# Performance work log

Hardware: AMD Instinct MI355X
Metric: run time of the kernel (lower is better)

The kernel has to match this reference:

```python
import jax, jax.numpy as jnp
import numpy as np

# ---- constants (match init_kwargs / input_specs) ----
B, NPG, EPG = 512, 50, 60          # graphs, nodes/graph, edges/graph
D, V = 128, 100000                 # embedding_dim, num_items
SPLITS, SCALE = 4, 12.0            # euler steps, logit scale
N, E = B * NPG, B * EPG
STDV = 1.0 / np.sqrt(D)


def _seg_sum(vals, idx, n):
    return jax.ops.segment_sum(vals, idx, num_segments=n)


def _l2norm(x, eps=1e-12):
    return x / jnp.maximum(jnp.linalg.norm(x, axis=-1, keepdims=True), eps)


def setup_inputs() -> dict:
    key = jax.random.key(0)
    ks = jax.random.split(key, 40)
    u = lambda i, shape: jax.random.uniform(ks[i], shape, minval=-STDV, maxval=STDV, dtype=jnp.float32)
    offs = jnp.repeat(jnp.arange(B, dtype=jnp.int32) * NPG, EPG)
    inp = dict(
        iid=jax.random.randint(ks[0], (N,), 0, V),
        src=jax.random.randint(ks[1], (E,), 0, NPG).astype(jnp.int32) + offs,
        dst=jax.random.randint(ks[2], (E,), 0, NPG).astype(jnp.int32) + offs,
        edge_w=jax.random.uniform(ks[3], (E,), minval=0.1, maxval=1.0, dtype=jnp.float32),
        edge_t=jax.random.uniform(ks[4], (E,), dtype=jnp.float32),
        node_t=jax.random.uniform(ks[5], (N,), dtype=jnp.float32),
        emb=u(6, (V, D)),
        # GGNN layer (num_layers=1): W1, W2 and torch-layout GRUCell(2D -> D)
        W1=u(7, (D, D)), W2=u(8, (D, D)),
        gw_ih=u(9, (3 * D, 2 * D)), gw_hh=u(10, (3 * D, D)),
        gb_ih=u(11, (3 * D,)), gb_hh=u(12, (3 * D,)),
        # GraphGRUODE GCNConv weights (x@W + b), norm='both'
        Wxr=u(13, (D, D)), bxr=u(14, (D,)), Wxz=u(15, (D, D)), bxz=u(16, (D,)),
        Wxh=u(17, (D, D)), bxh=u(18, (D,)), Whr=u(19, (D, D)), bhr=u(20, (D,)),
        Whz=u(21, (D, D)), bhz=u(22, (D,)), Whh=u(23, (D, D)), bhh=u(24, (D,)),
        # AttnReadout
        Wu=u(25, (D, D)), Wv=u(26, (D, D)), bv=u(27, (D,)), We=u(28, (D, 1)),
        # fc_sr: [2D -> D], no bias
        W_sr=u(29, (2 * D, D)),
    )
    return inp


def reference(iid, src, dst, edge_w, edge_t, node_t, emb,
              W1, W2, gw_ih, gw_hh, gb_ih, gb_hh,
              Wxr, bxr, Wxz, bxz, Wxh, bxh, Whr, bhr, Whz, bhz, Whh, bhh,
              Wu, Wv, bv, We, W_sr):
    # ---- embedding + normalize ----
    feat = _l2norm(emb[iid])                                   # [N, D]

    # ---- GGNNLayer: weighted mean over in-edges, both directions, GRU cell ----
    wcol = edge_w[:, None]
    num1 = _seg_sum(feat[src] * wcol, dst, N)
    den1 = _seg_sum(edge_w, dst, N)
    neigh1 = num1 / jnp.where(den1 == 0, 1.0, den1)[:, None]    # zero for isolated nodes
    num2 = _seg_sum(feat[dst] * wcol, src, N)
    den2 = _seg_sum(edge_w, src, N)
    neigh2 = num2 / jnp.where(den2 == 0, 1.0, den2)[:, None]
    hn = jnp.concatenate([neigh1 @ W1, neigh2 @ W2], axis=1)    # [N, 2D]
    gi = hn @ gw_ih.T + gb_ih
    gh = feat @ gw_hh.T + gb_hh
    ir, iz, ig = jnp.split(gi, 3, axis=1)
    hr, hz, hg = jnp.split(gh, 3, axis=1)
    r = jax.nn.sigmoid(ir + hr)
    z = jax.nn.sigmoid(iz + hz)
    g = jnp.tanh(ig + r * hg)
    feat = (1.0 - z) * g + z * feat
    feat = _l2norm(feat)

    # ---- GraphGRUODE: euler integration over dynamic masked subgraphs ----
    x = feat
    t_end = edge_t.max()
    dt = t_end / SPLITS
    nodiag = src != dst

    def ode_f(t, h):
        nm = node_t >= t                                        # node subgraph mask
        em = (edge_t <= t) & nm[src] & nm[dst] & nodiag          # edge mask (no self-loops)
        emf = em.astype(h.dtype)
        deg = _seg_sum(emf, src, N) + _seg_sum(emf, dst, N)      # undirected degree (reverse edges added)
        dis = jnp.clip(deg, 1.0, None) ** -0.5

        def conv(inp, W, b):                                     # GCNConv, norm='both'
            s = inp * dis[:, None]
            agg = (_seg_sum(s[src] * emf[:, None], dst, N)
                   + _seg_sum(s[dst] * emf[:, None], src, N))
            return (agg * dis[:, None]) @ W + b

        rr = jax.nn.sigmoid(conv(x, Wxr, bxr) + conv(h, Whr, bhr))
        zz = jax.nn.sigmoid(conv(x, Wxz, bxz) + conv(h, Whz, bhz))
        uu = jnp.tanh(conv(x, Wxh, bxh) + conv(rr * h, Whh, bhh))
        dh = (1.0 - zz) * (uu - h)
        return jnp.where(nm[:, None], dh, 0.0)

    h = x
    for k in range(SPLITS):
        h = h + dt * ode_f(k * dt, h)
    feat = _l2norm(h)

    # ---- AttnReadout (fixed NPG nodes/graph -> reshape as segment ops) ----
    fb = feat.reshape(B, NPG, D)
    last = fb[:, -1, :]                                          # last node of each session
    e = jax.nn.sigmoid(fb @ Wu + (last @ Wv + bv)[:, None, :]) @ We   # [B, NPG, 1]
    alpha = jax.nn.softmax(e, axis=1)
    sr_g = jnp.sum(fb * alpha, axis=1)                           # [B, D]

    sr = _l2norm(jnp.concatenate([last, sr_g], axis=1) @ W_sr)   # [B, D]
    target = _l2norm(emb)                                        # [V, D]
    logits = sr @ target.T                                       # [B, V]
    return jax.nn.log_softmax(SCALE * logits, axis=-1)
```

## Files before the change

kernel.cpp:

```cpp
#include <hip/hip_runtime.h>

#define BB 512
#define NPG 50
#define EPG 60
#define DD 128
#define VV 100000
#define VPAD 100032
#define NSPLITS 4
#define FSCALE 12.0f
#define NN (BB*NPG)
#define EE (BB*EPG)
#define NCB (VPAD/64)
#define HSTR 132
#define RSTR 136
#define TSTR 72
#define MSTR 72

typedef __attribute__((ext_vector_type(8))) short bfx8;
typedef __attribute__((ext_vector_type(4))) float f32x4;

__device__ __forceinline__ float sigmoidf_(float x){ return 1.f/(1.f+expf(-x)); }
__device__ __forceinline__ short f2bf(float f){
  union { float f; unsigned u; } v; v.f = f;
  unsigned r = v.u + 0x7FFF + ((v.u >> 16) & 1);
  return (short)(r >> 16);
}
__device__ __forceinline__ float bf2f(short s){
  union { unsigned u; float f; } v; v.u = ((unsigned)(unsigned short)s) << 16;
  return v.f;
}
__device__ __forceinline__ unsigned cvtpk_(float lo, float hi){
  unsigned r; asm("v_cvt_pk_bf16_f32 %0, %1, %2" : "=v"(r) : "v"(lo), "v"(hi)); return r;
}
__device__ __forceinline__ bfx8 pack8(float4 a, float4 b){
  union { bfx8 v; unsigned u[4]; } w;
  w.u[0] = cvtpk_(a.x, a.y); w.u[1] = cvtpk_(a.z, a.w);
  w.u[2] = cvtpk_(b.x, b.y); w.u[3] = cvtpk_(b.z, b.w);
  return w.v;
}

__global__ __launch_bounds__(256) void k_embn(const float* __restrict__ emb, short* __restrict__ embn) {
  int row = blockIdx.x*4 + (threadIdx.x >> 6);
  int lane = threadIdx.x & 63;
  if (row >= VPAD) return;
  if (row >= VV) { embn[(size_t)row*DD+lane]=0; embn[(size_t)row*DD+64+lane]=0; return; }
  const float* r = emb + (size_t)row*DD;
  float a = r[lane], b = r[lane+64];
  float s = a*a + b*b;
  for (int off=32; off; off>>=1) s += __shfl_down(s, off);
  s = __shfl(s, 0);
  float inv = 1.0f/fmaxf(sqrtf(s), 1e-12f);
  embn[(size_t)row*DD+lane]    = f2bf(a*inv);
  embn[(size_t)row*DD+64+lane] = f2bf(b*inv);
}

__global__ __launch_bounds__(128) void k_gather(const int* __restrict__ iid, const float* __restrict__ emb,
                                                float* __restrict__ x, short* __restrict__ xb) {
  int n = blockIdx.x, d = threadIdx.x;
  int v = iid[n];
  float e = emb[(size_t)v*DD + d];
  __shared__ float red2[2];
  float ss = e*e;
  for (int off=32; off; off>>=1) ss += __shfl_down(ss, off);
  if ((d & 63)==0) red2[d>>6] = ss;
  __syncthreads();
  float inv = 1.f/fmaxf(sqrtf(red2[0]+red2[1]), 1e-12f);
  float f = e*inv;
  x[(size_t)n*DD + d] = f;
  xb[(size_t)n*DD + d] = f2bf(f);
}

__global__ __launch_bounds__(256) void k_dt(const float* __restrict__ edge_t, float* __restrict__ dtp) {
  __shared__ float red[256];
  float m = -1e30f;
  for (int e = threadIdx.x; e < EE; e += 256) m = fmaxf(m, edge_t[e]);
  red[threadIdx.x] = m; __syncthreads();
  for (int s=128; s; s>>=1){ if ((int)threadIdx.x < s) red[threadIdx.x] = fmaxf(red[threadIdx.x], red[threadIdx.x+s]); __syncthreads(); }
  if (threadIdx.x==0) dtp[0] = red[0] / (float)NSPLITS;
}

__global__ void k_m12t(const float* __restrict__ W1, const float* __restrict__ W2,
                       const float* __restrict__ gw_ih, short* __restrict__ M12t) {
  int c = blockIdx.x, k = threadIdx.x;
  const float* Wrow = (k < 128) ? (W1 + (size_t)k*128) : (W2 + (size_t)(k-128)*128);
  const float* grow = gw_ih + (size_t)c*256 + ((k < 128) ? 0 : 128);
  float s = 0.f;
  for (int j = 0; j < 128; ++j) s += Wrow[j]*grow[j];
  M12t[(size_t)c*256 + k] = f2bf(s);
}
__global__ void k_bfcopy(const float* __restrict__ src, short* __restrict__ dst) {
  size_t i = (size_t)blockIdx.x*blockDim.x + threadIdx.x;
  dst[i] = f2bf(src[i]);
}
__global__ void k_whrzt(const float* __restrict__ Whr, const float* __restrict__ Whz,
                        short* __restrict__ Whrzt) {
  int c = blockIdx.x, k = threadIdx.x;
  float v = (c < 128) ? Whr[(size_t)k*128 + c] : Whz[(size_t)k*128 + (c-128)];
  Whrzt[(size_t)c*128 + k] = f2bf(v);
}
__global__ void k_w3t(const float* __restrict__ Wxr, const float* __restrict__ Wxz,
                      const float* __restrict__ Wxh, short* __restrict__ W3t) {
  int c = blockIdx.x, k = threadIdx.x;
  float v = (c < 128) ? Wxr[(size_t)k*128 + c]
          : (c < 256) ? Wxz[(size_t)k*128 + (c-128)]
                      : Wxh[(size_t)k*128 + (c-256)];
  W3t[(size_t)c*128 + k] = f2bf(v);
}
__global__ void k_wt128(const float* __restrict__ W, short* __restrict__ Wt) {
  int c = blockIdx.x, k = threadIdx.x;
  Wt[(size_t)c*128 + k] = f2bf(W[(size_t)k*128 + c]);
}
__global__ void k_build_bias(const float* __restrict__ bxr, const float* __restrict__ bhr,
                             const float* __restrict__ bxz, const float* __restrict__ bhz,
                             const float* __restrict__ bxh, const float* __restrict__ bhh,
                             float* __restrict__ brz, float* __restrict__ bu) {
  int t = threadIdx.x;
  if (t < 128) brz[t] = bxr[t] + bhr[t];
  else if (t < 256) brz[t] = bxz[t-128] + bhz[t-128];
  else bu[t-256] = bxh[t-256] + bhh[t-256];
}

__global__ __launch_bounds__(256) void k_grp_mean(const int* __restrict__ src, const int* __restrict__ dst,
                                                  const float* __restrict__ ew, const float* __restrict__ feat,
                                                  short* __restrict__ ABb) {
  __shared__ float fl[NPG*128];
  __shared__ float n1[NPG*128];
  __shared__ float n2[NPG*128];
  __shared__ int sl[EPG], tl[EPG];
  __shared__ float wl[EPG];
  __shared__ float d1[NPG], d2[NPG];
  int b = blockIdx.x, tid = threadIdx.x;
  int nb = b*NPG, eb = b*EPG;
  for (int i = tid; i < NPG*32; i += 256) {
    ((float4*)fl)[i] = ((const float4*)(feat + (size_t)nb*128))[i];
    ((float4*)n1)[i] = make_float4(0.f,0.f,0.f,0.f);
    ((float4*)n2)[i] = make_float4(0.f,0.f,0.f,0.f);
  }
  if (tid < EPG) { sl[tid] = src[eb+tid]-nb; tl[tid] = dst[eb+tid]-nb; wl[tid] = ew[eb+tid]; }
  __syncthreads();
  const int dgrp = tid >> 7, d = tid & 127;
  if (dgrp == 0) {
    for (int e = 0; e < EPG; ++e) n1[tl[e]*128+d] += fl[sl[e]*128+d]*wl[e];
  } else {
    for (int e = 0; e < EPG; ++e) n2[sl[e]*128+d] += fl[tl[e]*128+d]*wl[e];
  }
  if (tid < NPG) {
    float den = 0.f;
    for (int e = 0; e < EPG; ++e) den += (tl[e]==tid) ? wl[e] : 0.f;
    d1[tid] = (den == 0.f) ? 1.f : den;
  } else if (tid >= 128 && tid < 128+NPG) {
    int dd = tid - 128;
    float den = 0.f;
    for (int e = 0; e < EPG; ++e) den += (sl[e]==dd) ? wl[e] : 0.f;
    d2[dd] = (den == 0.f) ? 1.f : den;
  }
  __syncthreads();
  for (int n = 0; n < NPG; ++n) {
    float v = dgrp ? (n2[n*128+d]/d2[n]) : (n1[n*128+d]/d1[n]);
    ABb[(size_t)(nb+n)*256 + dgrp*128 + d] = f2bf(v);
  }
}

__global__ __launch_bounds__(128) void k_gru(const float* __restrict__ gi, const float* __restrict__ gh,
                                             float* __restrict__ x, short* __restrict__ xb2) {
  int n = blockIdx.x, d = threadIdx.x;
  const float* gin = gi + (size_t)n*384;
  const float* ghn = gh + (size_t)n*384;
  float ir = gin[d], iz = gin[128+d], ig = gin[256+d];
  float hr = ghn[d], hz = ghn[128+d], hg = ghn[256+d];
  float f0 = x[(size_t)n*DD + d];
  float r = sigmoidf_(ir + hr);
  float z = sigmoidf_(iz + hz);
  float g = tanhf(ig + r*hg);
  float f = (1.f - z)*g + z*f0;
  __shared__ float red2[2];
  float ss = f*f;
  for (int off=32; off; off>>=1) ss += __shfl_down(ss, off);
  if ((d & 63)==0) red2[d>>6] = ss;
  __syncthreads();
  float inv = 1.f/fmaxf(sqrtf(red2[0]+red2[1]), 1e-12f);
  float out = f*inv;
  x[(size_t)n*DD + d] = out;
  xb2[(size_t)n*DD + d] = f2bf(out);
}

__global__ __launch_bounds__(512, 4) void k_ode_fused(
    const int* __restrict__ src, const int* __restrict__ dst,
    const float* __restrict__ edge_t, const float* __restrict__ node_t,
    const float* __restrict__ dtp,
    float* __restrict__ x, short* __restrict__ fbb,
    const short* __restrict__ XA,
    const short* __restrict__ Whrzt, const short* __restrict__ Whht,
    const float* __restrict__ brz, const float* __restrict__ bu)
{
  __shared__ __align__(16) float hl[NPG*HSTR];
  __shared__ __align__(16) short rhb[NPG*RSTR];
  __shared__ __align__(16) short T1t[128*TSTR];
  __shared__ __align__(16) short Mp[64*MSTR];
  __shared__ int   rp[NPG+1];
  __shared__ short ci[2*EPG];
  __shared__ int   cnt[NPG];
  __shared__ int   stl[EPG];
  __shared__ float etl[EPG];
  __shared__ float ntl[NPG];
  __shared__ float disl[NPG];
  __shared__ unsigned long long actm_s;
  __shared__ float red8[8];

  const int b = blockIdx.x, tid = threadIdx.x;
  const int nb = b*NPG, eb = b*EPG;
  const int wave = tid>>6, lane = tid&63, quad = lane>>4, l16 = lane&15;
  const float dtv = dtp[0];

  for (int i = tid; i < NPG*32; i += 512) {
    int n = i >> 5, dq = i & 31;
    ((float4*)(hl + n*HSTR))[dq] = ((const float4*)(x + (size_t)(nb+n)*128))[dq];
  }
  if (tid < EPG) { stl[tid] = (src[eb+tid]-nb) | ((dst[eb+tid]-nb)<<16); etl[tid] = edge_t[eb+tid]; }
  if (tid >= 64 && tid < 64+NPG) ntl[tid-64] = node_t[nb+tid-64];
  __syncthreads();

  if (tid < NPG) {
    int c = 0;
    for (int e = 0; e < EPG; ++e) { int st=stl[e]; int s=st&0xffff, t=st>>16; c += (s==tid)+(t==tid); }
    cnt[tid] = c;
  }
  __syncthreads();
  if (tid == 0) { int a = 0; for (int n = 0; n < NPG; ++n) { rp[n] = a; a += cnt[n]; } rp[NPG] = a; }
  __syncthreads();
  if (tid < NPG) {
    int w = rp[tid];
    for (int e = 0; e < EPG; ++e) {
      int st = stl[e]; int s = st & 0xffff, t = st >> 16;
      if (t == tid) ci[w++] = (short)(s | (e<<8));
      if (s == tid) ci[w++] = (short)(t | (e<<8));
    }
  }
  __syncthreads();

  float zreg[4][4];

#define HW_PHASE(WT, XAOFS, USERH)                                                   \
  {                                                                                  \
    f32x4 acc[4] = {{0.f,0.f,0.f,0.f},{0.f,0.f,0.f,0.f},{0.f,0.f,0.f,0.f},{0.f,0.f,0.f,0.f}}; \
    const int coln = wave*16 + l16;                                                  \
    _Pragma("unroll")                                                                \
    for (int k0 = 0; k0 < 128; k0 += 32) {                                           \
      bfx8 af[4];                                                                    \
      _Pragma("unroll")                                                              \
      for (int m = 0; m < 4; ++m) {                                                  \
        int arow = m*16 + l16; if (arow > NPG-1) arow = NPG-1;                       \
        if (USERH) {                                                                 \
          af[m] = *(const bfx8*)&rhb[arow*RSTR + k0 + quad*8];                       \
        } else {                                                                     \
          const float* hp = &hl[arow*HSTR + k0 + quad*8];                            \
          float4 f0 = *(const float4*)hp;                                            \
          float4 f1 = *(const float4*)(hp+4);                                        \
          af[m] = pack8(f0, f1);                                                     \
        }                                                                            \
      }                                                                              \
      bfx8 bfr = *(const bfx8*)&(WT)[(size_t)coln*128 + k0 + quad*8];                \
      _Pragma("unroll")                                                              \
      for (int m = 0; m < 4; ++m)                                                    \
        acc[m] = __builtin_amdgcn_mfma_f32_16x16x32_bf16(af[m], bfr, acc[m], 0, 0, 0); \
    }                                                                                \
    _Pragma("unroll")                                                                \
    for (int m = 0; m < 4; ++m)                                                      \
      _Pragma("unroll")                                                              \
      for (int r = 0; r < 4; ++r) {                                                  \
        int row = m*16 + quad*4 + r;                                                 \
        int crow = (row > NPG-1) ? (NPG-1) : row;                                    \
        float v = acc[m][r] + bf2f(XA[(size_t)(nb+crow)*384 + (XAOFS) + coln]);      \
        T1t[coln*TSTR + row] = f2bf(v);                                              \
      }                                                                              \
  }

#define AGG_PHASE(WHICH)                                                             \
  {                                                                                  \
    f32x4 acc[4] = {{0.f,0.f,0.f,0.f},{0.f,0.f,0.f,0.f},{0.f,0.f,0.f,0.f},{0.f,0.f,0.f,0.f}}; \
    const int cold = wave*16 + l16;                                                  \
    _Pragma("unroll")                                                                \
    for (int k0 = 0; k0 < 64; k0 += 32) {                                            \
      bfx8 af[4];                                                                    \
      _Pragma("unroll")                                                              \
      for (int m = 0; m < 4; ++m) af[m] = *(const bfx8*)&Mp[(m*16+l16)*MSTR + k0 + quad*8]; \
      bfx8 bfr = *(const bfx8*)&T1t[cold*TSTR + k0 + quad*8];                        \
      _Pragma("unroll")                                                              \
      for (int m = 0; m < 4; ++m)                                                    \
        acc[m] = __builtin_amdgcn_mfma_f32_16x16x32_bf16(af[m], bfr, acc[m], 0, 0, 0); \
    }                                                                                \
    if ((WHICH) == 0) {                                                              \
      float bb = brz[cold];                                                          \
      _Pragma("unroll")                                                              \
      for (int m = 0; m < 4; ++m)                                                    \
        _Pragma("unroll")                                                            \
        for (int r = 0; r < 4; ++r) {                                                \
          int row = m*16 + quad*4 + r;                                               \
          if (row < NPG) {                                                           \
            float s = sigmoidf_(acc[m][r] + bb);                                     \
            rhb[row*RSTR + cold] = f2bf(s * hl[row*HSTR + cold]);                    \
          }                                                                          \
        }                                                                            \
    } else if ((WHICH) == 1) {                                                       \
      float bb = brz[128 + cold];                                                    \
      _Pragma("unroll")                                                              \
      for (int m = 0; m < 4; ++m)                                                    \
        _Pragma("unroll")                                                            \
        for (int r = 0; r < 4; ++r)                                                  \
          zreg[m][r] = sigmoidf_(acc[m][r] + bb);                                    \
    } else {                                                                         \
      float bb = bu[cold];                                                           \
      _Pragma("unroll")                                                              \
      for (int m = 0; m < 4; ++m)                                                    \
        _Pragma("unroll")                                                            \
        for (int r = 0; r < 4; ++r) {                                                \
          int row = m*16 + quad*4 + r;                                               \
          if (row < NPG && ntl[row] >= t) {                                          \
            float hv = hl[row*HSTR + cold];                                          \
            float uu = tanhf(acc[m][r] + bb);                                        \
            hl[row*HSTR + cold] = hv + dtv*(1.f - zreg[m][r])*(uu - hv);             \
          }                                                                          \
        }                                                                            \
    }                                                                                \
  }

  for (int ks = 0; ks < NSPLITS; ++ks) {
    const float t = (float)ks * dtv;
    if (wave == 0) {
      bool p = false;
      if (lane < EPG) {
        int st = stl[lane]; int s = st & 0xffff, tt = st >> 16;
        p = (etl[lane] <= t) && (ntl[s] >= t) && (ntl[tt] >= t) && (s != tt);
      }
      unsigned long long m = __ballot(p);
      if (lane == 0) actm_s = m;
    }
    for (int i = tid; i < 64*MSTR/2; i += 512) ((int*)Mp)[i] = 0;
    __syncthreads();
    const unsigned long long actm = actm_s;
    if (tid < NPG) {
      float deg = 0.f;
      for (int idx = rp[tid]; idx < rp[tid+1]; ++idx)
        deg += (float)((actm >> (((int)ci[idx]) >> 8)) & 1ULL);
      disl[tid] = rsqrtf(fmaxf(deg, 1.f));
    }
    __syncthreads();
    if (tid < NPG) {
      float dn = disl[tid];
      for (int idx = rp[tid]; idx < rp[tid+1]; ++idx) {
        int v = ci[idx]; int j = v & 255, e = v >> 8;
        if ((actm >> e) & 1ULL)
          Mp[tid*MSTR + j] = f2bf(bf2f(Mp[tid*MSTR + j]) + dn*disl[j]);
      }
    }
    __syncthreads();

    HW_PHASE(Whrzt, 0, false);            __syncthreads();
    AGG_PHASE(0);                         __syncthreads();
    HW_PHASE(Whrzt + 128*128, 128, false);__syncthreads();
    AGG_PHASE(1);                         __syncthreads();
    HW_PHASE(Whht, 256, true);            __syncthreads();
    AGG_PHASE(2);                         __syncthreads();
  }
#undef HW_PHASE
#undef AGG_PHASE

  for (int rr0 = 0; rr0 < NPG; rr0 += 4) {
    const int r = rr0 + (tid>>7);
    const int d = tid & 127;
    float v = (r < NPG) ? hl[r*HSTR + d] : 0.f;
    float ss = v*v;
    for (int off=32; off; off>>=1) ss += __shfl_down(ss, off);
    if (lane == 0) red8[wave] = ss;
    __syncthreads();
    int g = tid>>7;
    float inv = 1.f/fmaxf(sqrtf(red8[2*g]+red8[2*g+1]), 1e-12f);
    if (r < NPG) {
      float f = v*inv;
      x[(size_t)(nb+r)*128 + d] = f;
      fbb[(size_t)(nb+r)*128 + d] = f2bf(f);
    }
    __syncthreads();
  }
}

__global__ __launch_bounds__(256) void gemm_mfma(
    const short* __restrict__ A, int lda,
    const short* __restrict__ Bt, int ldbt,
    const float* __restrict__ bias,
    float* __restrict__ C, int ldc,
    int K, int mode,
    float* __restrict__ outp, float* __restrict__ pmax, float* __restrict__ psum)
{
  __shared__ short As[64*40];
  __shared__ short Bs[64*40];
  const int tid = threadIdx.x;
  const int wave = tid >> 6, lane = tid & 63;
  const int wr = wave >> 1, wc = wave & 1;
  const int quad = lane >> 4, l16 = lane & 15;
  int rb, cb;
  if (mode == 4 || mode == 5) {
    int t = (blockIdx.x & 7)*1563 + (blockIdx.x >> 3);
    rb = t & 7; cb = t >> 3;
  } else { rb = blockIdx.y; cb = blockIdx.x; }
  const int row0 = rb*64, col0 = cb*64;
  f32x4 acc[2][2] = {{{0.f,0.f,0.f,0.f},{0.f,0.f,0.f,0.f}},{{0.f,0.f,0.f,0.f},{0.f,0.f,0.f,0.f}}};
  const int sm = tid >> 2, skq = tid & 3;
  const short* Ap = A + (size_t)(row0+sm)*lda + skq*8;
  const short* Bp = Bt + (size_t)(col0+sm)*ldbt + skq*8;
  for (int k0 = 0; k0 < K; k0 += 32) {
    *(bfx8*)&As[sm*40 + skq*8] = *(const bfx8*)(Ap + k0);
    *(bfx8*)&Bs[sm*40 + skq*8] = *(const bfx8*)(Bp + k0);
    __syncthreads();
    bfx8 a0 = *(bfx8*)&As[(wr*32 + l16)*40 + quad*8];
    bfx8 a1 = *(bfx8*)&As[(wr*32 + 16 + l16)*40 + quad*8];
    bfx8 b0 = *(bfx8*)&Bs[(wc*32 + l16)*40 + quad*8];
    bfx8 b1 = *(bfx8*)&Bs[(wc*32 + 16 + l16)*40 + quad*8];
    acc[0][0] = __builtin_amdgcn_mfma_f32_16x16x32_bf16(a0, b0, acc[0][0], 0, 0, 0);
    acc[0][1] = __builtin_amdgcn_mfma_f32_16x16x32_bf16(a0, b1, acc[0][1], 0, 0, 0);
    acc[1][0] = __builtin_amdgcn_mfma_f32_16x16x32_bf16(a1, b0, acc[1][0], 0, 0, 0);
    acc[1][1] = __builtin_amdgcn_mfma_f32_16x16x32_bf16(a1, b1, acc[1][1], 0, 0, 0);
    __syncthreads();
  }

  if (mode == 0) {
#pragma unroll
    for (int i = 0; i < 2; ++i)
#pragma unroll
      for (int j = 0; j < 2; ++j) {
        int gc = col0 + wc*32 + j*16 + l16;
        float bb = bias ? bias[gc] : 0.f;
#pragma unroll
        for (int r = 0; r < 4; ++r) {
          int gr = row0 + wr*32 + i*16 + quad*4 + r;
          C[(size_t)gr*ldc + gc] = acc[i][j][r] + bb;
        }
      }
  } else if (mode == 6) {
    short* Cb = (short*)C;
#pragma unroll
    for (int i = 0; i < 2; ++i)
#pragma unroll
      for (int j = 0; j < 2; ++j) {
        int gc = col0 + wc*32 + j*16 + l16;
#pragma unroll
        for (int r = 0; r < 4; ++r) {
          int gr = row0 + wr*32 + i*16 + quad*4 + r;
          Cb[(size_t)gr*ldc + gc] = f2bf(acc[i][j][r]);
        }
      }
  } else if (mode == 4) {
    __shared__ float pm[64][2], ps[64][2];
    int c0 = col0 + wc*32 + l16;
    int c1 = c0 + 16;
#pragma unroll
    for (int i = 0; i < 2; ++i) {
#pragma unroll
      for (int r = 0; r < 4; ++r) {
        int rloc = wr*32 + i*16 + quad*4 + r;
        float v0 = (c0 < VV) ? acc[i][0][r] : -1e30f;
        float v1 = (c1 < VV) ? acc[i][1][r] : -1e30f;
        float m = fmaxf(v0, v1);
#pragma unroll
        for (int off = 1; off < 16; off <<= 1) m = fmaxf(m, __shfl_xor(m, off));
        float s = expf(v0 - m) + expf(v1 - m);
#pragma unroll
        for (int off = 1; off < 16; off <<= 1) s += __shfl_xor(s, off);
        if (l16 == 0) { pm[rloc][wc] = m; ps[rloc][wc] = s; }
      }
    }
    __syncthreads();
    if (tid < 64) {
      float m0 = pm[tid][0], m1 = pm[tid][1];
      float s0 = ps[tid][0], s1 = ps[tid][1];
      float M = fmaxf(m0, m1);
      float S = s0*expf(m0 - M) + s1*expf(m1 - M);
      pmax[(size_t)(row0 + tid)*NCB + cb] = M;
      psum[(size_t)(row0 + tid)*NCB + cb] = S;
    }
  } else {
#pragma unroll
    for (int i = 0; i < 2; ++i) {
#pragma unroll
      for (int r = 0; r < 4; ++r) {
        int gr = row0 + wr*32 + i*16 + quad*4 + r;
        float l = bias[gr];
#pragma unroll
        for (int j = 0; j < 2; ++j) {
          int gc = col0 + wc*32 + j*16 + l16;
          if (gc < VV) outp[(size_t)gr*VV + gc] = acc[i][j][r] - l;
        }
      }
    }
  }
}

__global__ __launch_bounds__(128) void k_attn(const float* __restrict__ fb, const float* __restrict__ U,
                                              const float* __restrict__ lv, const float* __restrict__ We,
                                              const float* __restrict__ W_sr, short* __restrict__ srvb) {
  int b = blockIdx.x, d = threadIdx.x;
  __shared__ float sc[NPG];
  __shared__ float lastv[DD], srg[DD];
  __shared__ float red2[2];
  const float* Ub  = U  + (size_t)b*NPG*DD;
  const float* lvb = lv + (size_t)b*DD;
  if (d < 64) {
    for (int i=0;i<NPG;++i) {
      float e = We[d]   * sigmoidf_(Ub[i*DD + d]      + lvb[d]) +
                We[d+64]* sigmoidf_(Ub[i*DD + 64 + d] + lvb[d+64]);
      for (int off=32; off; off>>=1) e += __shfl_down(e, off);
      if (d==0) sc[i] = e;
    }
  }
  __syncthreads();
  if (d < 64) {
    float v = (d < NPG) ? sc[d] : -1e30f;
    float m = v;
    for (int off=1; off<64; off<<=1) m = fmaxf(m, __shfl_xor(m, off));
    float ex = (d < NPG) ? expf(v - m) : 0.f;
    float s = ex;
    for (int off=1; off<64; off<<=1) s += __shfl_xor(s, off);
    if (d < NPG) sc[d] = ex/s;
  }
  __syncthreads();
  const float* fbb = fb + (size_t)b*NPG*DD;
  float lastd = fbb[(NPG-1)*DD + d];
  float sg = 0.f;
  for (int i=0;i<NPG;++i) sg += fbb[i*DD + d]*sc[i];
  lastv[d] = lastd; srg[d] = sg;
  __syncthreads();
  float acc = 0.f;
  for (int k=0;k<DD;++k) acc += lastv[k]*W_sr[k*DD + d];
  for (int k=0;k<DD;++k) acc += srg[k]*W_sr[(DD+k)*DD + d];
  float ss = acc*acc;
  for (int off=32; off; off>>=1) ss += __shfl_down(ss, off);
  if ((d & 63)==0) red2[d>>6] = ss;
  __syncthreads();
  float inv = 1.f/fmaxf(sqrtf(red2[0]+red2[1]), 1e-12f);
  srvb[(size_t)b*DD + d] = f2bf(FSCALE*acc*inv);
}

__global__ __launch_bounds__(256) void k_lse(const float* __restrict__ pmax, const float* __restrict__ psum,
                                             float* __restrict__ lse) {
  int r = blockIdx.x, tid = threadIdx.x;
  float m = -1e30f, s = 0.f;
  for (int cb = tid; cb < NCB; cb += 256) {
    float m2 = pmax[(size_t)r*NCB + cb], s2 = psum[(size_t)r*NCB + cb];
    float M = fmaxf(m, m2);
    s = s*expf(m - M) + s2*expf(m2 - M);
    m = M;
  }
  __shared__ float ms[256], ssh[256];
  ms[tid] = m; ssh[tid] = s; __syncthreads();
  for (int st=128; st; st>>=1) {
    if (tid < st) {
      float m2 = ms[tid+st], s2 = ssh[tid+st];
      float M = fmaxf(ms[tid], m2);
      ssh[tid] = ssh[tid]*expf(ms[tid]-M) + s2*expf(m2-M);
      ms[tid] = M;
    }
    __syncthreads();
  }
  if (tid==0) lse[r] = ms[0] + logf(ssh[0]);
}

extern "C" void kernel_launch(void* const* d_in, const int* in_sizes, int n_in,
                              void* d_out, int out_size, void* d_ws, size_t ws_size,
                              hipStream_t stream) {
  (void)in_sizes; (void)n_in; (void)out_size; (void)ws_size;
  const int*   iid    = (const int*)  d_in[0];
  const int*   src    = (const int*)  d_in[1];
  const int*   dst    = (const int*)  d_in[2];
  const float* edge_w = (const float*)d_in[3];
  const float* edge_t = (const float*)d_in[4];
  const float* node_t = (const float*)d_in[5];
  const float* emb    = (const float*)d_in[6];
  const float* W1     = (const float*)d_in[7];
  const float* W2     = (const float*)d_in[8];
  const float* gw_ih  = (const float*)d_in[9];
  const float* gw_hh  = (const float*)d_in[10];
  const float* gb_ih  = (const float*)d_in[11];
  const float* gb_hh  = (const float*)d_in[12];
  const float* Wxr = (const float*)d_in[13]; const float* bxr = (const float*)d_in[14];
  const float* Wxz = (const float*)d_in[15]; const float* bxz = (const float*)d_in[16];
  const float* Wxh = (const float*)d_in[17]; const float* bxh = (const float*)d_in[18];
  const float* Whr = (const float*)d_in[19]; const float* bhr = (const float*)d_in[20];
  const float* Whz = (const float*)d_in[21]; const float* bhz = (const float*)d_in[22];
  const float* Whh = (const float*)d_in[23]; const float* bhh = (const float*)d_in[24];
  const float* Wu  = (const float*)d_in[25];
  const float* Wv  = (const float*)d_in[26]; const float* bv  = (const float*)d_in[27];
  const float* We  = (const float*)d_in[28];
  const float* W_sr= (const float*)d_in[29];

  float* ws  = (float*)d_ws;
  float* out = (float*)d_out;

  short* embn  = (short*)ws;
  float* pmax  = ws + 6402048;
  float* psum  = pmax + 800256;
  short* M12t  = (short*)(ws + 8002560);
  short* gwhhb = (short*)(ws + 8051712);
  short* Whrzt = (short*)(ws + 8076288);
  short* Whht  = (short*)(ws + 8092672);
  short* W3t   = (short*)(ws + 8100864);
  short* Wut   = (short*)(ws + 8125440);
  short* Wvt   = (short*)(ws + 8133632);
  float* brz   = ws + 8141824;
  float* bu    = brz + 256;
  float* lv    = bu + 128;
  float* dtp   = lv + 65536;
  float* lse   = dtp + 4;
  short* srvb  = (short*)(lse + 512);

  short* ABb = (short*)out;
  float* x   = out + (size_t) 4*1024*1024;
  short* XA  = (short*)(out + (size_t) 8*1024*1024);
  float* gi  = out + (size_t)20*1024*1024;
  float* gh  = out + (size_t)30*1024*1024;
  float* U   = out + (size_t)20*1024*1024;
  short* xb  = (short*)(out + (size_t)40*1024*1024);
  short* xb2 = (short*)(out + (size_t)44*1024*1024);
  short* fbb = (short*)(out + (size_t)46*1024*1024);

  k_embn<<<VPAD/4, 256, 0, stream>>>(emb, embn);
  k_gather<<<NN, 128, 0, stream>>>(iid, emb, x, xb);
  k_dt<<<1, 256, 0, stream>>>(edge_t, dtp);
  k_m12t<<<384, 256, 0, stream>>>(W1, W2, gw_ih, M12t);
  k_bfcopy<<<384, 128, 0, stream>>>(gw_hh, gwhhb);
  k_whrzt<<<256, 128, 0, stream>>>(Whr, Whz, Whrzt);
  k_wt128<<<128, 128, 0, stream>>>(Whh, Whht);
  k_w3t<<<384, 128, 0, stream>>>(Wxr, Wxz, Wxh, W3t);
  k_wt128<<<128, 128, 0, stream>>>(Wu, Wut);
  k_wt128<<<128, 128, 0, stream>>>(Wv, Wvt);
  k_build_bias<<<1, 384, 0, stream>>>(bxr, bhr, bxz, bhz, bxh, bhh, brz, bu);

  k_grp_mean<<<BB, 256, 0, stream>>>(src, dst, edge_w, x, ABb);

  gemm_mfma<<<dim3(6,400), 256, 0, stream>>>(ABb, 256, M12t, 256, gb_ih, gi, 384, 256, 0,
      nullptr, nullptr, nullptr);
  gemm_mfma<<<dim3(6,400), 256, 0, stream>>>(xb, 128, gwhhb, 128, gb_hh, gh, 384, 128, 0,
      nullptr, nullptr, nullptr);
  k_gru<<<NN, 128, 0, stream>>>(gi, gh, x, xb2);

  gemm_mfma<<<dim3(6,400), 256, 0, stream>>>(xb2, 128, W3t, 128, nullptr, (float*)XA, 384, 128, 6,
      nullptr, nullptr, nullptr);

  k_ode_fused<<<BB, 512, 0, stream>>>(src, dst, edge_t, node_t, dtp, x, fbb, XA, Whrzt, Whht, brz, bu);

  gemm_mfma<<<dim3(2,400), 256, 0, stream>>>(fbb, 128, Wut, 128, nullptr, U, 128, 128, 0,
      nullptr, nullptr, nullptr);
  gemm_mfma<<<dim3(2,8), 256, 0, stream>>>(fbb + (size_t)(NPG-1)*DD, NPG*DD, Wvt, 128, bv, lv, 128, 128, 0,
      nullptr, nullptr, nullptr);
  k_attn<<<BB, 128, 0, stream>>>(x, U, lv, We, W_sr, srvb);

  gemm_mfma<<<dim3(8*NCB), 256, 0, stream>>>(srvb, 128, embn, 128, nullptr, nullptr, 0, 128, 4,
      nullptr, pmax, psum);
  k_lse<<<BB, 256, 0, stream>>>(pmax, psum, lse);
  gemm_mfma<<<dim3(8*NCB), 256, 0, stream>>>(srvb, 128, embn, 128, lse, nullptr, 0, 128, 5,
      out, nullptr, nullptr);
}
```

Measured before the change: 709.9 us.

## Fuse attention readout into ODE kernel, merge prep kernels, MFMA-based group mean

Merges the many small weight-preparation kernels and the dt reduction into one multi-role prep launch. Rewrites the group-mean aggregation as a dense 64x64 normalized adjacency matrix multiplied by the transposed features with bf16 MFMA, replacing the serial per-edge scatter. Fuses the attention readout (Wu/Wv projections, softmax, weighted sum, fc_sr and normalization) into the tail of the ODE kernel using the final h kept in LDS. This removes the global round-trips for fbb, U and lv plus several launches. It also stages XA tiles into LDS before each HW phase. In exchange the ODE kernel uses more LDS and registers, and the group mean now goes through bf16 rounding.

```diff
diff --git a/kernel.cpp b/kernel.cpp
--- a/kernel.cpp
+++ b/kernel.cpp
@@ -15,6 +15,7 @@
 #define RSTR 136
 #define TSTR 72
 #define MSTR 72
+#define FTSTR 72
 
 typedef __attribute__((ext_vector_type(8))) short bfx8;
 typedef __attribute__((ext_vector_type(4))) float f32x4;
@@ -70,94 +71,133 @@
   xb[(size_t)n*DD + d] = f2bf(f);
 }
 
-__global__ __launch_bounds__(256) void k_dt(const float* __restrict__ edge_t, float* __restrict__ dtp) {
-  __shared__ float red[256];
-  float m = -1e30f;
-  for (int e = threadIdx.x; e < EE; e += 256) m = fmaxf(m, edge_t[e]);
-  red[threadIdx.x] = m; __syncthreads();
-  for (int s=128; s; s>>=1){ if ((int)threadIdx.x < s) red[threadIdx.x] = fmaxf(red[threadIdx.x], red[threadIdx.x+s]); __syncthreads(); }
-  if (threadIdx.x==0) dtp[0] = red[0] / (float)NSPLITS;
-}
-
-__global__ void k_m12t(const float* __restrict__ W1, const float* __restrict__ W2,
-                       const float* __restrict__ gw_ih, short* __restrict__ M12t) {
-  int c = blockIdx.x, k = threadIdx.x;
-  const float* Wrow = (k < 128) ? (W1 + (size_t)k*128) : (W2 + (size_t)(k-128)*128);
-  const float* grow = gw_ih + (size_t)c*256 + ((k < 128) ? 0 : 128);
-  float s = 0.f;
-  for (int j = 0; j < 128; ++j) s += Wrow[j]*grow[j];
-  M12t[(size_t)c*256 + k] = f2bf(s);
-}
-__global__ void k_bfcopy(const float* __restrict__ src, short* __restrict__ dst) {
-  size_t i = (size_t)blockIdx.x*blockDim.x + threadIdx.x;
-  dst[i] = f2bf(src[i]);
-}
-__global__ void k_whrzt(const float* __restrict__ Whr, const float* __restrict__ Whz,
-                        short* __restrict__ Whrzt) {
-  int c = blockIdx.x, k = threadIdx.x;
-  float v = (c < 128) ? Whr[(size_t)k*128 + c] : Whz[(size_t)k*128 + (c-128)];
-  Whrzt[(size_t)c*128 + k] = f2bf(v);
-}
-__global__ void k_w3t(const float* __restrict__ Wxr, const float* __restrict__ Wxz,
-                      const float* __restrict__ Wxh, short* __restrict__ W3t) {
-  int c = blockIdx.x, k = threadIdx.x;
-  float v = (c < 128) ? Wxr[(size_t)k*128 + c]
-          : (c < 256) ? Wxz[(size_t)k*128 + (c-128)]
-                      : Wxh[(size_t)k*128 + (c-256)];
-  W3t[(size_t)c*128 + k] = f2bf(v);
-}
-__global__ void k_wt128(const float* __restrict__ W, short* __restrict__ Wt) {
-  int c = blockIdx.x, k = threadIdx.x;
-  Wt[(size_t)c*128 + k] = f2bf(W[(size_t)k*128 + c]);
-}
-__global__ void k_build_bias(const float* __restrict__ bxr, const float* __restrict__ bhr,
-                             const float* __restrict__ bxz, const float* __restrict__ bhz,
-                             const float* __restrict__ bxh, const float* __restrict__ bhh,
-                             float* __restrict__ brz, float* __restrict__ bu) {
-  int t = threadIdx.x;
-  if (t < 128) brz[t] = bxr[t] + bhr[t];
-  else if (t < 256) brz[t] = bxz[t-128] + bhz[t-128];
-  else bu[t-256] = bxh[t-256] + bhh[t-256];
-}
-
-__global__ __launch_bounds__(256) void k_grp_mean(const int* __restrict__ src, const int* __restrict__ dst,
+__global__ __launch_bounds__(256) void k_prep(
+    const float* __restrict__ W1, const float* __restrict__ W2, const float* __restrict__ gw_ih,
+    const float* __restrict__ gw_hh,
+    const float* __restrict__ Whr, const float* __restrict__ Whz, const float* __restrict__ Whh,
+    const float* __restrict__ Wxr, const float* __restrict__ Wxz, const float* __restrict__ Wxh,
+    const float* __restrict__ Wu, const float* __restrict__ Wv,
+    const float* __restrict__ bxr, const float* __restrict__ bhr,
+    const float* __restrict__ bxz, const float* __restrict__ bhz,
+    const float* __restrict__ bxh, const float* __restrict__ bhh,
+    const float* __restrict__ edge_t,
+    short* __restrict__ M12t, short* __restrict__ gwhhb,
+    short* __restrict__ Whrzt, short* __restrict__ Whht, short* __restrict__ W3t,
+    short* __restrict__ Wut, short* __restrict__ Wvt,
+    float* __restrict__ brz, float* __restrict__ bu, float* __restrict__ dtp)
+{
+  const int blk = blockIdx.x, tid = threadIdx.x;
+  if (blk < 384) {
+    int c = blk, k = tid;
+    const float* Wrow = (k < 128) ? (W1 + (size_t)k*128) : (W2 + (size_t)(k-128)*128);
+    const float* grow = gw_ih + (size_t)c*256 + ((k < 128) ? 0 : 128);
+    float s = 0.f;
+    for (int j = 0; j < 128; ++j) s += Wrow[j]*grow[j];
+    M12t[(size_t)c*256 + k] = f2bf(s);
+  } else if (blk < 576) {
+    int i = (blk-384)*256 + tid;
+    gwhhb[i] = f2bf(gw_hh[i]);
+  } else if (blk < 704) {
+    int c = ((blk-576)<<1) | (tid>>7), k = tid & 127;
+    float v = (c < 128) ? Whr[(size_t)k*128+c] : Whz[(size_t)k*128+(c-128)];
+    Whrzt[(size_t)c*128 + k] = f2bf(v);
+  } else if (blk < 768) {
+    int c = ((blk-704)<<1) | (tid>>7), k = tid & 127;
+    Whht[(size_t)c*128 + k] = f2bf(Whh[(size_t)k*128 + c]);
+  } else if (blk < 960) {
+    int c = ((blk-768)<<1) | (tid>>7), k = tid & 127;
+    float v = (c < 128) ? Wxr[(size_t)k*128 + c]
+            : (c < 256) ? Wxz[(size_t)k*128 + (c-128)]
+                        : Wxh[(size_t)k*128 + (c-256)];
+    W3t[(size_t)c*128 + k] = f2bf(v);
+  } else if (blk < 1024) {
+    int c = ((blk-960)<<1) | (tid>>7), k = tid & 127;
+    Wut[(size_t)c*128 + k] = f2bf(Wu[(size_t)k*128 + c]);
+  } else if (blk < 1088) {
+    int c = ((blk-1024)<<1) | (tid>>7), k = tid & 127;
+    Wvt[(size_t)c*128 + k] = f2bf(Wv[(size_t)k*128 + c]);
+  } else if (blk == 1088) {
+    for (int t = tid; t < 384; t += 256) {
+      if (t < 128) brz[t] = bxr[t] + bhr[t];
+      else if (t < 256) brz[t] = bxz[t-128] + bhz[t-128];
+      else bu[t-256] = bxh[t-256] + bhh[t-256];
+    }
+  } else {
+    __shared__ float red[256];
+    float m = -1e30f;
+    for (int e = tid; e < EE; e += 256) m = fmaxf(m, edge_t[e]);
+    red[tid] = m; __syncthreads();
+    for (int s=128; s; s>>=1){ if (tid < s) red[tid] = fmaxf(red[tid], red[tid+s]); __syncthreads(); }
+    if (tid==0) dtp[0] = red[0] / (float)NSPLITS;
+  }
+}
+
+__global__ __launch_bounds__(512) void k_grp_mean(const int* __restrict__ src, const int* __restrict__ dst,
                                                   const float* __restrict__ ew, const float* __restrict__ feat,
                                                   short* __restrict__ ABb) {
-  __shared__ float fl[NPG*128];
-  __shared__ float n1[NPG*128];
-  __shared__ float n2[NPG*128];
-  __shared__ int sl[EPG], tl[EPG];
+  __shared__ __align__(16) short featT[128*FTSTR];
+  __shared__ __align__(16) float Mwf[2][64*64];
+  __shared__ __align__(16) short Mw[2][64*MSTR];
+  __shared__ float den[2][64];
+  __shared__ int stl[EPG];
   __shared__ float wl[EPG];
-  __shared__ float d1[NPG], d2[NPG];
-  int b = blockIdx.x, tid = threadIdx.x;
-  int nb = b*NPG, eb = b*EPG;
-  for (int i = tid; i < NPG*32; i += 256) {
-    ((float4*)fl)[i] = ((const float4*)(feat + (size_t)nb*128))[i];
-    ((float4*)n1)[i] = make_float4(0.f,0.f,0.f,0.f);
-    ((float4*)n2)[i] = make_float4(0.f,0.f,0.f,0.f);
-  }
-  if (tid < EPG) { sl[tid] = src[eb+tid]-nb; tl[tid] = dst[eb+tid]-nb; wl[tid] = ew[eb+tid]; }
-  __syncthreads();
-  const int dgrp = tid >> 7, d = tid & 127;
-  if (dgrp == 0) {
-    for (int e = 0; e < EPG; ++e) n1[tl[e]*128+d] += fl[sl[e]*128+d]*wl[e];
-  } else {
-    for (int e = 0; e < EPG; ++e) n2[sl[e]*128+d] += fl[tl[e]*128+d]*wl[e];
-  }
+  const int b = blockIdx.x, tid = threadIdx.x;
+  const int nb = b*NPG, eb = b*EPG;
+  const int wave = tid>>6, lane = tid&63, quad = lane>>4, l16 = lane&15;
+  if (tid < EPG) { stl[tid] = (src[eb+tid]-nb) | ((dst[eb+tid]-nb)<<16); wl[tid] = ew[eb+tid]; }
+  for (int i = tid; i < 64*32; i += 512) {
+    int n = i >> 5, fq = i & 31;
+    float4 v = (n < NPG) ? ((const float4*)(feat + (size_t)(nb+n)*128))[fq] : make_float4(0.f,0.f,0.f,0.f);
+    featT[(fq*4+0)*FTSTR + n] = f2bf(v.x);
+    featT[(fq*4+1)*FTSTR + n] = f2bf(v.y);
+    featT[(fq*4+2)*FTSTR + n] = f2bf(v.z);
+    featT[(fq*4+3)*FTSTR + n] = f2bf(v.w);
+  }
+  for (int i = tid; i < 2*64*64; i += 512) ((float*)Mwf)[i] = 0.f;
+  if (tid < 128) den[tid>>6][tid&63] = 1.f;
+  __syncthreads();
   if (tid < NPG) {
-    float den = 0.f;
-    for (int e = 0; e < EPG; ++e) den += (tl[e]==tid) ? wl[e] : 0.f;
-    d1[tid] = (den == 0.f) ? 1.f : den;
-  } else if (tid >= 128 && tid < 128+NPG) {
-    int dd = tid - 128;
-    float den = 0.f;
-    for (int e = 0; e < EPG; ++e) den += (sl[e]==dd) ? wl[e] : 0.f;
-    d2[dd] = (den == 0.f) ? 1.f : den;
-  }
-  __syncthreads();
-  for (int n = 0; n < NPG; ++n) {
-    float v = dgrp ? (n2[n*128+d]/d2[n]) : (n1[n*128+d]/d1[n]);
-    ABb[(size_t)(nb+n)*256 + dgrp*128 + d] = f2bf(v);
+    float dA = 0.f;
+    for (int e = 0; e < EPG; ++e) {
+      int st = stl[e]; int s = st & 0xffff, t = st >> 16;
+      if (t == tid) { Mwf[0][tid*64 + s] += wl[e]; dA += wl[e]; }
+    }
+    den[0][tid] = (dA == 0.f) ? 1.f : dA;
+  } else if (tid >= 64 && tid < 64+NPG) {
+    int n = tid - 64; float dB = 0.f;
+    for (int e = 0; e < EPG; ++e) {
+      int st = stl[e]; int s = st & 0xffff, t = st >> 16;
+      if (s == n) { Mwf[1][n*64 + t] += wl[e]; dB += wl[e]; }
+    }
+    den[1][n] = (dB == 0.f) ? 1.f : dB;
+  }
+  __syncthreads();
+  for (int i = tid; i < 2*64*64; i += 512) {
+    int q = i >> 12, rr = (i >> 6) & 63, j = i & 63;
+    Mw[q][rr*MSTR + j] = f2bf(Mwf[q][rr*64 + j] / den[q][rr]);
+  }
+  __syncthreads();
+#pragma unroll
+  for (int q = 0; q < 2; ++q) {
+    f32x4 acc[4] = {{0.f,0.f,0.f,0.f},{0.f,0.f,0.f,0.f},{0.f,0.f,0.f,0.f},{0.f,0.f,0.f,0.f}};
+    const int coln = wave*16 + l16;
+#pragma unroll
+    for (int k0 = 0; k0 < 64; k0 += 32) {
+      bfx8 af[4];
+#pragma unroll
+      for (int m = 0; m < 4; ++m) af[m] = *(const bfx8*)&Mw[q][(m*16+l16)*MSTR + k0 + quad*8];
+      bfx8 bfr = *(const bfx8*)&featT[coln*FTSTR + k0 + quad*8];
+#pragma unroll
+      for (int m = 0; m < 4; ++m)
+        acc[m] = __builtin_amdgcn_mfma_f32_16x16x32_bf16(af[m], bfr, acc[m], 0, 0, 0);
+    }
+#pragma unroll
+    for (int m = 0; m < 4; ++m)
+#pragma unroll
+      for (int r = 0; r < 4; ++r) {
+        int row = m*16 + quad*4 + r;
+        if (row < NPG) ABb[(size_t)(nb+row)*256 + q*128 + coln] = f2bf(acc[m][r]);
+      }
   }
 }
 
@@ -188,10 +228,13 @@
     const int* __restrict__ src, const int* __restrict__ dst,
     const float* __restrict__ edge_t, const float* __restrict__ node_t,
     const float* __restrict__ dtp,
-    float* __restrict__ x, short* __restrict__ fbb,
+    const float* __restrict__ x,
     const short* __restrict__ XA,
     const short* __restrict__ Whrzt, const short* __restrict__ Whht,
-    const float* __restrict__ brz, const float* __restrict__ bu)
+    const float* __restrict__ brz, const float* __restrict__ bu,
+    const short* __restrict__ Wut, const short* __restrict__ Wvt,
+    const float* __restrict__ bv, const float* __restrict__ We_,
+    const float* __restrict__ W_sr, short* __restrict__ srvb)
 {
   __shared__ __align__(16) float hl[NPG*HSTR];
   __shared__ __align__(16) short rhb[NPG*RSTR];
@@ -204,6 +247,9 @@
   __shared__ float etl[EPG];
   __shared__ float ntl[NPG];
   __shared__ float disl[NPG];
+  __shared__ float lvl[DD];
+  __shared__ float srgl[DD];
+  __shared__ float scl[NPG];
   __shared__ unsigned long long actm_s;
   __shared__ float red8[8];
 
@@ -242,6 +288,14 @@
 
 #define HW_PHASE(WT, XAOFS, USERH)                                                   \
   {                                                                                  \
+    for (int i = tid; i < 64*16; i += 512) {                                         \
+      int row = i >> 4, cq = i & 15;                                                 \
+      int crow = (row > NPG-1) ? (NPG-1) : row;                                      \
+      bfx8 v = *(const bfx8*)&XA[(size_t)(nb+crow)*384 + (XAOFS) + cq*8];            \
+      _Pragma("unroll")                                                              \
+      for (int j = 0; j < 8; ++j) T1t[(cq*8+j)*TSTR + row] = v[j];                   \
+    }                                                                                \
+    __syncthreads();                                                                 \
     f32x4 acc[4] = {{0.f,0.f,0.f,0.f},{0.f,0.f,0.f,0.f},{0.f,0.f,0.f,0.f},{0.f,0.f,0.f,0.f}}; \
     const int coln = wave*16 + l16;                                                  \
     _Pragma("unroll")                                                                \
@@ -254,9 +308,7 @@
           af[m] = *(const bfx8*)&rhb[arow*RSTR + k0 + quad*8];                       \
         } else {                                                                     \
           const float* hp = &hl[arow*HSTR + k0 + quad*8];                            \
-          float4 f0 = *(const float4*)hp;                                            \
-          float4 f1 = *(const float4*)(hp+4);                                        \
-          af[m] = pack8(f0, f1);                                                     \
+          af[m] = pack8(*(const float4*)hp, *(const float4*)(hp+4));                 \
         }                                                                            \
       }                                                                              \
       bfx8 bfr = *(const bfx8*)&(WT)[(size_t)coln*128 + k0 + quad*8];                \
@@ -269,8 +321,7 @@
       _Pragma("unroll")                                                              \
       for (int r = 0; r < 4; ++r) {                                                  \
         int row = m*16 + quad*4 + r;                                                 \
-        int crow = (row > NPG-1) ? (NPG-1) : row;                                    \
-        float v = acc[m][r] + bf2f(XA[(size_t)(nb+crow)*384 + (XAOFS) + coln]);      \
+        float v = acc[m][r] + bf2f(T1t[coln*TSTR + row]);                            \
         T1t[coln*TSTR + row] = f2bf(v);                                              \
       }                                                                              \
   }
@@ -375,12 +426,78 @@
     __syncthreads();
     int g = tid>>7;
     float inv = 1.f/fmaxf(sqrtf(red8[2*g]+red8[2*g+1]), 1e-12f);
-    if (r < NPG) {
-      float f = v*inv;
-      x[(size_t)(nb+r)*128 + d] = f;
-      fbb[(size_t)(nb+r)*128 + d] = f2bf(f);
-    }
-    __syncthreads();
+    if (r < NPG) hl[r*HSTR + d] = v*inv;
+    __syncthreads();
+  }
+
+  {
+    f32x4 acc[4] = {{0.f,0.f,0.f,0.f},{0.f,0.f,0.f,0.f},{0.f,0.f,0.f,0.f},{0.f,0.f,0.f,0.f}};
+    const int coln = wave*16 + l16;
+#pragma unroll
+    for (int k0 = 0; k0 < 128; k0 += 32) {
+      bfx8 af[4];
+#pragma unroll
+      for (int m = 0; m < 4; ++m) {
+        int arow = m*16 + l16; if (arow > NPG-1) arow = NPG-1;
+        const float* hp = &hl[arow*HSTR + k0 + quad*8];
+        af[m] = pack8(*(const float4*)hp, *(const float4*)(hp+4));
+      }
+      bfx8 bfr = *(const bfx8*)&Wut[(size_t)coln*128 + k0 + quad*8];
+#pragma unroll
+      for (int m = 0; m < 4; ++m)
+        acc[m] = __builtin_amdgcn_mfma_f32_16x16x32_bf16(af[m], bfr, acc[m], 0, 0, 0);
+    }
+#pragma unroll
+    for (int m = 0; m < 4; ++m)
+#pragma unroll
+      for (int r = 0; r < 4; ++r) {
+        int row = m*16 + quad*4 + r;
+        if (row < NPG) rhb[row*RSTR + coln] = f2bf(acc[m][r]);
+      }
+  }
+  __syncthreads();
+  if (tid < 128) {
+    float a = bv[tid];
+    for (int k = 0; k < 128; ++k) a += hl[(NPG-1)*HSTR + k] * bf2f(Wvt[(size_t)tid*128 + k]);
+    lvl[tid] = a;
+  }
+  __syncthreads();
+  for (int i = wave; i < NPG; i += 8) {
+    int d0 = lane, d1 = lane + 64;
+    float e = We_[d0]*sigmoidf_(bf2f(rhb[i*RSTR + d0]) + lvl[d0])
+            + We_[d1]*sigmoidf_(bf2f(rhb[i*RSTR + d1]) + lvl[d1]);
+    for (int off=32; off; off>>=1) e += __shfl_down(e, off);
+    if (lane == 0) scl[i] = e;
+  }
+  __syncthreads();
+  if (wave == 0) {
+    float v = (lane < NPG) ? scl[lane] : -1e30f;
+    float m = v;
+    for (int off=1; off<64; off<<=1) m = fmaxf(m, __shfl_xor(m, off));
+    float ex = (lane < NPG) ? expf(v - m) : 0.f;
+    float s = ex;
+    for (int off=1; off<64; off<<=1) s += __shfl_xor(s, off);
+    if (lane < NPG) scl[lane] = ex/s;
+  }
+  __syncthreads();
+  if (tid < 128) {
+    float sg = 0.f;
+    for (int i = 0; i < NPG; ++i) sg += hl[i*HSTR + tid] * scl[i];
+    srgl[tid] = sg;
+  }
+  __syncthreads();
+  float accv = 0.f;
+  if (tid < 128) {
+    for (int k = 0; k < 128; ++k) accv += hl[(NPG-1)*HSTR + k] * W_sr[(size_t)k*128 + tid];
+    for (int k = 0; k < 128; ++k) accv += srgl[k] * W_sr[(size_t)(128+k)*128 + tid];
+    float ss = accv*accv;
+    for (int off=32; off; off>>=1) ss += __shfl_down(ss, off);
+    if (lane == 0) red8[wave] = ss;
+  }
+  __syncthreads();
+  if (tid < 128) {
+    float inv = 1.f/fmaxf(sqrtf(red8[0]+red8[1]), 1e-12f);
+    srvb[(size_t)b*DD + tid] = f2bf(FSCALE*accv*inv);
   }
 }
 
@@ -495,51 +612,6 @@
   }
 }
 
-__global__ __launch_bounds__(128) void k_attn(const float* __restrict__ fb, const float* __restrict__ U,
-                                              const float* __restrict__ lv, const float* __restrict__ We,
-                                              const float* __restrict__ W_sr, short* __restrict__ srvb) {
-  int b = blockIdx.x, d = threadIdx.x;
-  __shared__ float sc[NPG];
-  __shared__ float lastv[DD], srg[DD];
-  __shared__ float red2[2];
-  const float* Ub  = U  + (size_t)b*NPG*DD;
-  const float* lvb = lv + (size_t)b*DD;
-  if (d < 64) {
-    for (int i=0;i<NPG;++i) {
-      float e = We[d]   * sigmoidf_(Ub[i*DD + d]      + lvb[d]) +
-                We[d+64]* sigmoidf_(Ub[i*DD + 64 + d] + lvb[d+64]);
-      for (int off=32; off; off>>=1) e += __shfl_down(e, off);
-      if (d==0) sc[i] = e;
-    }
-  }
-  __syncthreads();
-  if (d < 64) {
-    float v = (d < NPG) ? sc[d] : -1e30f;
-    float m = v;
-    for (int off=1; off<64; off<<=1) m = fmaxf(m, __shfl_xor(m, off));
-    float ex = (d < NPG) ? expf(v - m) : 0.f;
-    float s = ex;
-    for (int off=1; off<64; off<<=1) s += __shfl_xor(s, off);
-    if (d < NPG) sc[d] = ex/s;
-  }
-  __syncthreads();
-  const float* fbb = fb + (size_t)b*NPG*DD;
-  float lastd = fbb[(NPG-1)*DD + d];
-  float sg = 0.f;
-  for (int i=0;i<NPG;++i) sg += fbb[i*DD + d]*sc[i];
-  lastv[d] = lastd; srg[d] = sg;
-  __syncthreads();
-  float acc = 0.f;
-  for (int k=0;k<DD;++k) acc += lastv[k]*W_sr[k*DD + d];
-  for (int k=0;k<DD;++k) acc += srg[k]*W_sr[(DD+k)*DD + d];
-  float ss = acc*acc;
-  for (int off=32; off; off>>=1) ss += __shfl_down(ss, off);
-  if ((d & 63)==0) red2[d>>6] = ss;
-  __syncthreads();
-  float inv = 1.f/fmaxf(sqrtf(red2[0]+red2[1]), 1e-12f);
-  srvb[(size_t)b*DD + d] = f2bf(FSCALE*acc*inv);
-}
-
 __global__ __launch_bounds__(256) void k_lse(const float* __restrict__ pmax, const float* __restrict__ psum,
                                              float* __restrict__ lse) {
   int r = blockIdx.x, tid = threadIdx.x;
@@ -607,8 +679,7 @@
   short* Wvt   = (short*)(ws + 8133632);
   float* brz   = ws + 8141824;
   float* bu    = brz + 256;
-  float* lv    = bu + 128;
-  float* dtp   = lv + 65536;
+  float* dtp   = bu + 128;
   float* lse   = dtp + 4;
   short* srvb  = (short*)(lse + 512);
 
@@ -617,24 +688,16 @@
   short* XA  = (short*)(out + (size_t) 8*1024*1024);
   float* gi  = out + (size_t)20*1024*1024;
   float* gh  = out + (size_t)30*1024*1024;
-  float* U   = out + (size_t)20*1024*1024;
   short* xb  = (short*)(out + (size_t)40*1024*1024);
   short* xb2 = (short*)(out + (size_t)44*1024*1024);
-  short* fbb = (short*)(out + (size_t)46*1024*1024);
-
+
+  k_prep<<<1090, 256, 0, stream>>>(W1, W2, gw_ih, gw_hh, Whr, Whz, Whh, Wxr, Wxz, Wxh, Wu, Wv,
+      bxr, bhr, bxz, bhz, bxh, bhh, edge_t,
+      M12t, gwhhb, Whrzt, Whht, W3t, Wut, Wvt, brz, bu, dtp);
   k_embn<<<VPAD/4, 256, 0, stream>>>(emb, embn);
   k_gather<<<NN, 128, 0, stream>>>(iid, emb, x, xb);
-  k_dt<<<1, 256, 0, stream>>>(edge_t, dtp);
-  k_m12t<<<384, 256, 0, stream>>>(W1, W2, gw_ih, M12t);
-  k_bfcopy<<<384, 128, 0, stream>>>(gw_hh, gwhhb);
-  k_whrzt<<<256, 128, 0, stream>>>(Whr, Whz, Whrzt);
-  k_wt128<<<128, 128, 0, stream>>>(Whh, Whht);
-  k_w3t<<<384, 128, 0, stream>>>(Wxr, Wxz, Wxh, W3t);
-  k_wt128<<<128, 128, 0, stream>>>(Wu, Wut);
-  k_wt128<<<128, 128, 0, stream>>>(Wv, Wvt);
-  k_build_bias<<<1, 384, 0, stream>>>(bxr, bhr, bxz, bhz, bxh, bhh, brz, bu);
-
-  k_grp_mean<<<BB, 256, 0, stream>>>(src, dst, edge_w, x, ABb);
+
+  k_grp_mean<<<BB, 512, 0, stream>>>(src, dst, edge_w, x, ABb);
 
   gemm_mfma<<<dim3(6,400), 256, 0, stream>>>(ABb, 256, M12t, 256, gb_ih, gi, 384, 256, 0,
       nullptr, nullptr, nullptr);
@@ -645,13 +708,8 @@
   gemm_mfma<<<dim3(6,400), 256, 0, stream>>>(xb2, 128, W3t, 128, nullptr, (float*)XA, 384, 128, 6,
       nullptr, nullptr, nullptr);
 
-  k_ode_fused<<<BB, 512, 0, stream>>>(src, dst, edge_t, node_t, dtp, x, fbb, XA, Whrzt, Whht, brz, bu);
-
-  gemm_mfma<<<dim3(2,400), 256, 0, stream>>>(fbb, 128, Wut, 128, nullptr, U, 128, 128, 0,
-      nullptr, nullptr, nullptr);
-  gemm_mfma<<<dim3(2,8), 256, 0, stream>>>(fbb + (size_t)(NPG-1)*DD, NPG*DD, Wvt, 128, bv, lv, 128, 128, 0,
-      nullptr, nullptr, nullptr);
-  k_attn<<<BB, 128, 0, stream>>>(x, U, lv, We, W_sr, srvb);
+  k_ode_fused<<<BB, 512, 0, stream>>>(src, dst, edge_t, node_t, dtp, x, XA, Whrzt, Whht, brz, bu,
+      Wut, Wvt, bv, We, W_sr, srvb);
 
   gemm_mfma<<<dim3(8*NCB), 256, 0, stream>>>(srvb, 128, embn, 128, nullptr, nullptr, 0, 128, 4,
       nullptr, pmax, psum);
```

Measured after the change: 655.3 us. -7.7%, faster.
